# Kernel tuning notes

Measured on AMD Instinct MI355X. Metric: run time of the kernel, lower is better.

The kernel has to match this reference:

```python
import jax, jax.numpy as jnp
import numpy as np

N_NODES = 50000
N_EDGES = 640000
HIDDEN = 128


def setup_inputs() -> dict:
    key = jax.random.key(0)
    ks = jax.random.split(key, 8)
    z = jax.random.normal(ks[0], (N_NODES, HIDDEN), dtype=jnp.float32)
    sources = jax.random.randint(ks[1], (N_EDGES,), 0, N_NODES)
    dists = jax.random.randint(ks[2], (N_EDGES,), 0, N_NODES)
    weights = jax.random.uniform(ks[3], (N_EDGES, 1), dtype=jnp.float32)
    # nn.Linear-style params: W has shape [out, in]; we store transposed [in, out]
    s_msg = 1.0 / np.sqrt(2 * HIDDEN + 1)
    W_msg = jax.random.uniform(ks[4], (2 * HIDDEN + 1, HIDDEN), minval=-s_msg, maxval=s_msg, dtype=jnp.float32)
    b_msg = jax.random.uniform(ks[5], (HIDDEN,), minval=-s_msg, maxval=s_msg, dtype=jnp.float32)
    s_upd = 1.0 / np.sqrt(2 * HIDDEN)
    W_upd = jax.random.uniform(ks[6], (2 * HIDDEN, HIDDEN), minval=-s_upd, maxval=s_upd, dtype=jnp.float32)
    b_upd = jax.random.uniform(ks[7], (HIDDEN,), minval=-s_upd, maxval=s_upd, dtype=jnp.float32)
    return {"z": z, "sources": sources, "dists": dists, "weights": weights,
            "W_msg": W_msg, "b_msg": b_msg, "W_upd": W_upd, "b_upd": b_upd}


def reference(z, sources, dists, weights, W_msg, b_msg, W_upd, b_upd):
    n = z.shape[0]
    # gather -> concat -> message linear: [E, 2h+1] @ [2h+1, h]
    msg_input = jnp.concatenate([z[sources], z[dists], weights], axis=1)
    messages = msg_input @ W_msg + b_msg
    # scatter-amax aggregate into node buffers (empty nodes -> -inf -> 0)
    agg = jax.ops.segment_max(messages, dists, num_segments=n)
    agg = jnp.where(jnp.isinf(agg), 0.0, agg)
    # update linear on [n, 2h]
    return jnp.concatenate([z, agg], axis=1) @ W_upd + b_upd
```

## Files before the change

### kernel.cpp

```cpp
#include <hip/hip_runtime.h>

#define H 128
#define KSLOT 64
#define CSTRIDE 16

typedef __attribute__((ext_vector_type(8))) short bf8;
typedef __attribute__((ext_vector_type(8))) unsigned short u16x8;
typedef __attribute__((ext_vector_type(4))) float f32x4;

__device__ __forceinline__ unsigned short f2bf(float f) {
    unsigned u = __float_as_uint(f);
    return (unsigned short)((u + 0x7FFFu + ((u >> 16) & 1u)) >> 16);
}
__device__ __forceinline__ float bf2f(unsigned short b) {
    return __uint_as_float(((unsigned)b) << 16);
}

__global__ __launch_bounds__(256) void prep(
    const float* __restrict__ z, const float* __restrict__ Wmsg, const float* __restrict__ Wupd,
    unsigned short* __restrict__ zb,
    unsigned short* __restrict__ WmT,
    unsigned short* __restrict__ WuT,
    int* __restrict__ cnt,
    unsigned short* __restrict__ ZS,
    int N)
{
    const int t = blockIdx.x * 256 + threadIdx.x;
    const int n4 = (N * CSTRIDE) >> 2;
    if (t < n4) ((int4*)cnt)[t] = make_int4(0, 0, 0, 0);
    const int zi = t * 8;
    if (zi < N * H) {
        const float4* p = (const float4*)(z + zi);
        float4 v0 = p[0], v1 = p[1];
        ushort4 o0, o1;
        o0.x = f2bf(v0.x); o0.y = f2bf(v0.y); o0.z = f2bf(v0.z); o0.w = f2bf(v0.w);
        o1.x = f2bf(v1.x); o1.y = f2bf(v1.y); o1.z = f2bf(v1.z); o1.w = f2bf(v1.w);
        ushort4* q = (ushort4*)(zb + zi);
        q[0] = o0; q[1] = o1;
    }
    if (t < 16) {
        u16x8 s;
#pragma unroll
        for (int i = 0; i < 8; ++i) s[i] = 0xFF80;
        *(u16x8*)(ZS + (size_t)N * H + t * 8) = s;
    }
    if (t < 256 * H) {
        const int c = t >> 7, k = t & 127;
        WmT[t] = f2bf(Wmsg[(size_t)(k + (c & 128)) * H + (c & 127)]);
    }
    if (t < H * 256) {
        const int c = t >> 8, k = t & 255;
        WuT[t] = f2bf(Wupd[(size_t)k * H + c]);
    }
}

__global__ __launch_bounds__(256) void gemm1_scatter(
    const unsigned short* __restrict__ zb,
    const unsigned short* __restrict__ WmT,
    unsigned short* __restrict__ ZS,
    unsigned short* __restrict__ ZD,
    const int* __restrict__ src, const int* __restrict__ dst,
    const float* __restrict__ wgt, int* __restrict__ cnt,
    int2* __restrict__ ew,
    int N, int E, int ntiles, int ngemm)
{
    if ((int)blockIdx.x >= ngemm) {
        const int base = (blockIdx.x - ngemm) * 1024 + threadIdx.x;
        int dv[4], sv[4]; float wv[4]; bool ok[4];
#pragma unroll
        for (int k = 0; k < 4; ++k) {
            const int e = base + k * 256;
            ok[k] = e < E;
            const int ec = ok[k] ? e : 0;
            dv[k] = dst[ec]; sv[k] = src[ec]; wv[k] = wgt[ec];
        }
#pragma unroll
        for (int k = 0; k < 4; ++k) {
            if (ok[k]) {
                int p = atomicAdd(&cnt[(size_t)dv[k] * CSTRIDE], 1);
                if (p < KSLOT)
                    ew[((size_t)dv[k] << 6) + p] = make_int2(sv[k], __float_as_int(wv[k]));
            }
        }
        return;
    }
    const int l = threadIdx.x & 63;
    const int w = threadIdx.x >> 6;
    const int r = l & 15, g = l >> 4;
    const int colbase = w * 64;
    unsigned short* Out = (w < 2) ? ZS : ZD;
    const int outcol = colbase & 127;

    bf8 wf[4][4];
#pragma unroll
    for (int nf = 0; nf < 4; ++nf)
#pragma unroll
        for (int kk = 0; kk < 4; ++kk)
            wf[kk][nf] = *(const bf8*)(WmT + (size_t)(colbase + nf * 16 + r) * H + kk * 32 + g * 8);

    const f32x4 zero = {0.f, 0.f, 0.f, 0.f};
    for (int tt = blockIdx.x; tt < ntiles; tt += ngemm) {
        const int row0 = tt * 32;
#pragma unroll
        for (int m = 0; m < 2; ++m) {
            const int node = row0 + m * 16 + r;
            const int rowc = node < N ? node : N - 1;
            bf8 zf[4];
#pragma unroll
            for (int kk = 0; kk < 4; ++kk)
                zf[kk] = *(const bf8*)(zb + (size_t)rowc * H + kk * 32 + g * 8);
            f32x4 acc[4] = {zero, zero, zero, zero};
#pragma unroll
            for (int kk = 0; kk < 4; ++kk)
#pragma unroll
                for (int nf = 0; nf < 4; ++nf)
                    acc[nf] = __builtin_amdgcn_mfma_f32_16x16x32_bf16(wf[kk][nf], zf[kk], acc[nf], 0, 0, 0);
            if (node < N) {
#pragma unroll
                for (int nf = 0; nf < 4; ++nf) {
                    ushort4 o;
                    o.x = f2bf(acc[nf][0]); o.y = f2bf(acc[nf][1]);
                    o.z = f2bf(acc[nf][2]); o.w = f2bf(acc[nf][3]);
                    *(ushort4*)(Out + (size_t)node * H + outcol + nf * 16 + g * 4) = o;
                }
            }
        }
    }
}

__global__ __launch_bounds__(256) void aggregate(
    const unsigned short* __restrict__ ZS,
    const unsigned short* __restrict__ ZD,
    unsigned short* __restrict__ Agg,
    const float* __restrict__ bmsg, const float* __restrict__ wrow,
    const int* __restrict__ cnt, const int2* __restrict__ ew, int N)
{
    const int node = blockIdx.x * 4 + (threadIdx.x >> 6);
    if (node >= N) return;
    const int l = threadIdx.x & 63;
    const int sub = l >> 4;
    const int c16 = l & 15;

    const int d = min(cnt[(size_t)node * CSTRIDE], KSLOT);
    const int iters = (d + 7) >> 3;

    float wr[8];
    {
        float4 w0 = *(const float4*)(wrow + c16 * 8);
        float4 w1 = *(const float4*)(wrow + c16 * 8 + 4);
        wr[0] = w0.x; wr[1] = w0.y; wr[2] = w0.z; wr[3] = w0.w;
        wr[4] = w1.x; wr[5] = w1.y; wr[6] = w1.z; wr[7] = w1.w;
    }

    const float NINF = -__builtin_inff();
    float m[8];
#pragma unroll
    for (int i = 0; i < 8; ++i) m[i] = NINF;

    const int2* ep = ew + ((size_t)node << 6) + sub;
#pragma unroll 2
    for (int j = 0; j < iters; ++j) {
        const int s0 = j * 8 + sub, s1 = s0 + 4;
        int2 e0 = ep[j * 8];
        int2 e1 = ep[j * 8 + 4];
        const int r0 = (s0 < d) ? e0.x : N;
        const int r1 = (s1 < d) ? e1.x : N;
        const float w0 = (s0 < d) ? __int_as_float(e0.y) : 0.f;
        const float w1 = (s1 < d) ? __int_as_float(e1.y) : 0.f;
        u16x8 v0 = *(const u16x8*)(ZS + (size_t)r0 * H + c16 * 8);
        u16x8 v1 = *(const u16x8*)(ZS + (size_t)r1 * H + c16 * 8);
#pragma unroll
        for (int i = 0; i < 8; ++i)
            m[i] = fmaxf(m[i], __builtin_fmaf(w0, wr[i], bf2f((unsigned short)v0[i])));
#pragma unroll
        for (int i = 0; i < 8; ++i)
            m[i] = fmaxf(m[i], __builtin_fmaf(w1, wr[i], bf2f((unsigned short)v1[i])));
    }
#pragma unroll
    for (int i = 0; i < 8; ++i) {
        m[i] = fmaxf(m[i], __shfl_xor(m[i], 16));
        m[i] = fmaxf(m[i], __shfl_xor(m[i], 32));
    }

    if (sub == 0) {
        u16x8 zd = *(const u16x8*)(ZD + (size_t)node * H + c16 * 8);
        float bm[8];
        float4 b0 = *(const float4*)(bmsg + c16 * 8);
        float4 b1 = *(const float4*)(bmsg + c16 * 8 + 4);
        bm[0] = b0.x; bm[1] = b0.y; bm[2] = b0.z; bm[3] = b0.w;
        bm[4] = b1.x; bm[5] = b1.y; bm[6] = b1.z; bm[7] = b1.w;
        u16x8 o;
#pragma unroll
        for (int i = 0; i < 8; ++i) {
            float r = (d > 0) ? (m[i] + bf2f((unsigned short)zd[i]) + bm[i]) : 0.f;
            o[i] = f2bf(r);
        }
        *(u16x8*)(Agg + (size_t)node * H + c16 * 8) = o;
    }
}

__global__ __launch_bounds__(256) void gemm_upd_mfma(
    const unsigned short* __restrict__ zb,
    const unsigned short* __restrict__ Agg,
    const unsigned short* __restrict__ WuT,
    const float* __restrict__ bupd,
    float* __restrict__ out, int N, int ntiles)
{
    const int l = threadIdx.x & 63;
    const int w = threadIdx.x >> 6;
    const int r = l & 15, g = l >> 4;
    const int colbase = w * 32;

    bf8 wf[8][2];
#pragma unroll
    for (int nf = 0; nf < 2; ++nf)
#pragma unroll
        for (int kk = 0; kk < 8; ++kk)
            wf[kk][nf] = *(const bf8*)(WuT + (size_t)(colbase + nf * 16 + r) * 256 + kk * 32 + g * 8);
    float4 bias[2];
#pragma unroll
    for (int nf = 0; nf < 2; ++nf)
        bias[nf] = *(const float4*)(bupd + colbase + nf * 16 + g * 4);

    const f32x4 zero = {0.f, 0.f, 0.f, 0.f};
    for (int tt = blockIdx.x; tt < ntiles; tt += gridDim.x) {
        const int row0 = tt * 32;
#pragma unroll
        for (int m = 0; m < 2; ++m) {
            const int node = row0 + m * 16 + r;
            const int rowc = node < N ? node : N - 1;
            bf8 zf[8];
#pragma unroll
            for (int kk = 0; kk < 4; ++kk)
                zf[kk] = *(const bf8*)(zb + (size_t)rowc * H + kk * 32 + g * 8);
#pragma unroll
            for (int kk = 4; kk < 8; ++kk)
                zf[kk] = *(const bf8*)(Agg + (size_t)rowc * H + (kk - 4) * 32 + g * 8);
            f32x4 acc[2] = {zero, zero};
#pragma unroll
            for (int kk = 0; kk < 8; ++kk)
#pragma unroll
                for (int nf = 0; nf < 2; ++nf)
                    acc[nf] = __builtin_amdgcn_mfma_f32_16x16x32_bf16(wf[kk][nf], zf[kk], acc[nf], 0, 0, 0);
            if (node < N) {
#pragma unroll
                for (int nf = 0; nf < 2; ++nf) {
                    float4 o;
                    o.x = acc[nf][0] + bias[nf].x;
                    o.y = acc[nf][1] + bias[nf].y;
                    o.z = acc[nf][2] + bias[nf].z;
                    o.w = acc[nf][3] + bias[nf].w;
                    *(float4*)(out + (size_t)node * H + colbase + nf * 16 + g * 4) = o;
                }
            }
        }
    }
}

extern "C" void kernel_launch(void* const* d_in, const int* in_sizes, int n_in,
                              void* d_out, int out_size, void* d_ws, size_t ws_size,
                              hipStream_t stream) {
    const float* z    = (const float*)d_in[0];
    const int*   src  = (const int*)d_in[1];
    const int*   dst  = (const int*)d_in[2];
    const float* wgt  = (const float*)d_in[3];
    const float* Wmsg = (const float*)d_in[4];
    const float* bmsg = (const float*)d_in[5];
    const float* Wupd = (const float*)d_in[6];
    const float* bupd = (const float*)d_in[7];
    float* out = (float*)d_out;

    const int N = in_sizes[0] / H;
    const int E = in_sizes[1];
    const int Npad = ((N + 31) / 32) * 32;
    const int ntiles = Npad / 32;

    unsigned short* zb  = (unsigned short*)d_ws;
    unsigned short* ZS  = zb + (size_t)Npad * H;
    unsigned short* ZD  = ZS + (size_t)(Npad + 32) * H;
    unsigned short* Agg = ZD + (size_t)Npad * H;
    unsigned short* WmT = Agg + (size_t)Npad * H;
    unsigned short* WuT = WmT + 256 * H;
    int*  cnt = (int*)(WuT + H * 256);
    int2* ew  = (int2*)(cnt + (size_t)N * CSTRIDE);

    const int ngemm = 784;
    const int nscat = (E + 1023) / 1024;
    const int nprep_threads = max(N * H / 8, (N * CSTRIDE) / 4);
    const int nprep = (nprep_threads + 255) / 256;

    prep<<<nprep, 256, 0, stream>>>(z, Wmsg, Wupd, zb, WmT, WuT, cnt, ZS, N);

    gemm1_scatter<<<ngemm + nscat, 256, 0, stream>>>(
        zb, WmT, ZS, ZD, src, dst, wgt, cnt, ew, N, E, ntiles, ngemm);

    aggregate<<<(N + 3) / 4, 256, 0, stream>>>(
        ZS, ZD, Agg, bmsg, Wmsg + (size_t)256 * H, cnt, ew, N);

    gemm_upd_mfma<<<784, 256, 0, stream>>>(zb, Agg, WuT, bupd, out, N, ntiles);
}
```

Baseline: 117.9 us.

## Replace per-node atomic slot scatter with counting-sort edge partition and LDS tile aggregation

The per-node atomic counter and fixed 64-slot edge buckets are replaced by a chunked histogram over 64-node tiles, split into 4 sub-bins by node index modulo 4. Two scan kernels and a partition kernel then write the edges into a compact sorted array, packing the source index and local destination into one int. A tile_agg kernel has each wave walk its sub-bin and keep per-node maxima in shared memory before applying the bias and the ZD term. This removes the global atomics, the per-node degree cap and the sentinel row, in exchange for four extra launches, a one-block scan, and narrower 4-byte gathers with fewer edges in flight per wave.

Measured after the change: 152.0 us. 1.29x slower.

```diff
diff --git a/kernel.cpp b/kernel.cpp
--- a/kernel.cpp
+++ b/kernel.cpp
@@ -1,8 +1,8 @@
 #include <hip/hip_runtime.h>
 
 #define H 128
-#define KSLOT 64
-#define CSTRIDE 16
+#define CHUNK 4096
+#define MAXB 3200
 
 typedef __attribute__((ext_vector_type(8))) short bf8;
 typedef __attribute__((ext_vector_type(8))) unsigned short u16x8;
@@ -21,13 +21,9 @@
     unsigned short* __restrict__ zb,
     unsigned short* __restrict__ WmT,
     unsigned short* __restrict__ WuT,
-    int* __restrict__ cnt,
-    unsigned short* __restrict__ ZS,
     int N)
 {
     const int t = blockIdx.x * 256 + threadIdx.x;
-    const int n4 = (N * CSTRIDE) >> 2;
-    if (t < n4) ((int4*)cnt)[t] = make_int4(0, 0, 0, 0);
     const int zi = t * 8;
     if (zi < N * H) {
         const float4* p = (const float4*)(z + zi);
@@ -38,12 +34,6 @@
         ushort4* q = (ushort4*)(zb + zi);
         q[0] = o0; q[1] = o1;
     }
-    if (t < 16) {
-        u16x8 s;
-#pragma unroll
-        for (int i = 0; i < 8; ++i) s[i] = 0xFF80;
-        *(u16x8*)(ZS + (size_t)N * H + t * 8) = s;
-    }
     if (t < 256 * H) {
         const int c = t >> 7, k = t & 127;
         WmT[t] = f2bf(Wmsg[(size_t)(k + (c & 128)) * H + (c & 127)]);
@@ -54,36 +44,13 @@
     }
 }
 
-__global__ __launch_bounds__(256) void gemm1_scatter(
+__global__ __launch_bounds__(256) void gemm1(
     const unsigned short* __restrict__ zb,
     const unsigned short* __restrict__ WmT,
     unsigned short* __restrict__ ZS,
     unsigned short* __restrict__ ZD,
-    const int* __restrict__ src, const int* __restrict__ dst,
-    const float* __restrict__ wgt, int* __restrict__ cnt,
-    int2* __restrict__ ew,
-    int N, int E, int ntiles, int ngemm)
-{
-    if ((int)blockIdx.x >= ngemm) {
-        const int base = (blockIdx.x - ngemm) * 1024 + threadIdx.x;
-        int dv[4], sv[4]; float wv[4]; bool ok[4];
-#pragma unroll
-        for (int k = 0; k < 4; ++k) {
-            const int e = base + k * 256;
-            ok[k] = e < E;
-            const int ec = ok[k] ? e : 0;
-            dv[k] = dst[ec]; sv[k] = src[ec]; wv[k] = wgt[ec];
-        }
-#pragma unroll
-        for (int k = 0; k < 4; ++k) {
-            if (ok[k]) {
-                int p = atomicAdd(&cnt[(size_t)dv[k] * CSTRIDE], 1);
-                if (p < KSLOT)
-                    ew[((size_t)dv[k] << 6) + p] = make_int2(sv[k], __float_as_int(wv[k]));
-            }
-        }
-        return;
-    }
+    int N, int ntiles)
+{
     const int l = threadIdx.x & 63;
     const int w = threadIdx.x >> 6;
     const int r = l & 15, g = l >> 4;
@@ -99,7 +66,7 @@
             wf[kk][nf] = *(const bf8*)(WmT + (size_t)(colbase + nf * 16 + r) * H + kk * 32 + g * 8);
 
     const f32x4 zero = {0.f, 0.f, 0.f, 0.f};
-    for (int tt = blockIdx.x; tt < ntiles; tt += ngemm) {
+    for (int tt = blockIdx.x; tt < ntiles; tt += gridDim.x) {
         const int row0 = tt * 32;
 #pragma unroll
         for (int m = 0; m < 2; ++m) {
@@ -128,74 +95,161 @@
     }
 }
 
-__global__ __launch_bounds__(256) void aggregate(
+__global__ __launch_bounds__(256) void hist_tiles(
+    const int* __restrict__ dst, int* __restrict__ histG, int E, int NT4)
+{
+    __shared__ int h[MAXB];
+    for (int i = threadIdx.x; i < NT4; i += 256) h[i] = 0;
+    __syncthreads();
+    const int e0 = blockIdx.x * CHUNK;
+#pragma unroll
+    for (int j = 0; j < CHUNK / 256; ++j) {
+        const int e = e0 + j * 256 + threadIdx.x;
+        if (e < E) {
+            const int d = dst[e];
+            atomicAdd(&h[(d >> 6) * 4 + (d & 3)], 1);
+        }
+    }
+    __syncthreads();
+    for (int i = threadIdx.x; i < NT4; i += 256)
+        histG[(size_t)blockIdx.x * NT4 + i] = h[i];
+}
+
+__global__ __launch_bounds__(256) void scan_bins(
+    int* __restrict__ histG, int* __restrict__ tileTot, int NB, int NT4)
+{
+    __shared__ int sh[256];
+    const int b = blockIdx.x;
+    const int t = threadIdx.x;
+    int v = (t < NB) ? histG[(size_t)t * NT4 + b] : 0;
+    sh[t] = v;
+    __syncthreads();
+#pragma unroll
+    for (int off = 1; off < 256; off <<= 1) {
+        int x = (t >= off) ? sh[t - off] : 0;
+        __syncthreads();
+        sh[t] += x;
+        __syncthreads();
+    }
+    if (t < NB) histG[(size_t)t * NT4 + b] = sh[t] - v;
+    if (t == 255) tileTot[b] = sh[255];
+}
+
+__global__ __launch_bounds__(256) void scan_total(
+    const int* __restrict__ tileTot, int* __restrict__ tileBase, int NT4)
+{
+    __shared__ int sh[256];
+    const int t = threadIdx.x;
+    const int PER = (NT4 + 255) / 256;
+    int loc[16];
+    int s = 0;
+    for (int j = 0; j < PER; ++j) {
+        const int i = t * PER + j;
+        const int v = (i < NT4) ? tileTot[i] : 0;
+        loc[j] = s; s += v;
+    }
+    sh[t] = s;
+    __syncthreads();
+#pragma unroll
+    for (int off = 1; off < 256; off <<= 1) {
+        int x = (t >= off) ? sh[t - off] : 0;
+        __syncthreads();
+        sh[t] += x;
+        __syncthreads();
+    }
+    const int base = sh[t] - s;
+    for (int j = 0; j < PER; ++j) {
+        const int i = t * PER + j;
+        if (i < NT4) tileBase[i] = base + loc[j];
+    }
+}
+
+__global__ __launch_bounds__(256) void partition_edges(
+    const int* __restrict__ src, const int* __restrict__ dst, const float* __restrict__ wgt,
+    const int* __restrict__ histG, const int* __restrict__ tileBase,
+    int2* __restrict__ EP, int E, int NT4)
+{
+    __shared__ int c[MAXB];
+    for (int i = threadIdx.x; i < NT4; i += 256) c[i] = 0;
+    __syncthreads();
+    const int e0 = blockIdx.x * CHUNK;
+    const size_t hbase = (size_t)blockIdx.x * NT4;
+#pragma unroll
+    for (int j = 0; j < CHUNK / 256; ++j) {
+        const int e = e0 + j * 256 + threadIdx.x;
+        if (e < E) {
+            const int d = dst[e];
+            const int b = (d >> 6) * 4 + (d & 3);
+            const int r = atomicAdd(&c[b], 1);
+            const int slot = tileBase[b] + histG[hbase + b] + r;
+            EP[slot] = make_int2(src[e] | ((d & 63) << 16), __float_as_int(wgt[e]));
+        }
+    }
+}
+
+__global__ __launch_bounds__(256) void tile_agg(
     const unsigned short* __restrict__ ZS,
     const unsigned short* __restrict__ ZD,
     unsigned short* __restrict__ Agg,
     const float* __restrict__ bmsg, const float* __restrict__ wrow,
-    const int* __restrict__ cnt, const int2* __restrict__ ew, int N)
-{
-    const int node = blockIdx.x * 4 + (threadIdx.x >> 6);
-    if (node >= N) return;
-    const int l = threadIdx.x & 63;
-    const int sub = l >> 4;
-    const int c16 = l & 15;
-
-    const int d = min(cnt[(size_t)node * CSTRIDE], KSLOT);
-    const int iters = (d + 7) >> 3;
-
-    float wr[8];
-    {
-        float4 w0 = *(const float4*)(wrow + c16 * 8);
-        float4 w1 = *(const float4*)(wrow + c16 * 8 + 4);
-        wr[0] = w0.x; wr[1] = w0.y; wr[2] = w0.z; wr[3] = w0.w;
-        wr[4] = w1.x; wr[5] = w1.y; wr[6] = w1.z; wr[7] = w1.w;
-    }
-
+    const int* __restrict__ tileBase, const int* __restrict__ tileTot,
+    const int2* __restrict__ EP, int N)
+{
+    __shared__ float agg[64][132];
+    const int t = blockIdx.x;
+    const int w = threadIdx.x >> 6;
+    const int lane = threadIdx.x & 63;
+
+    for (int i = threadIdx.x; i < 64 * 132; i += 256)
+        ((float*)agg)[i] = -__builtin_inff();
+    __syncthreads();
+
+    const float wr0 = wrow[2 * lane], wr1 = wrow[2 * lane + 1];
+    const int b = t * 4 + w;
+    int p = tileBase[b];
+    const int pe = p + tileTot[b];
+
+#define PROC(rr, qq)                                                         \
+    {                                                                        \
+        const int dl = (rr.x >> 16) & 63;                                    \
+        const float ww = __int_as_float(rr.y);                               \
+        const float v0 = __builtin_fmaf(ww, wr0, bf2f((unsigned short)(qq & 0xFFFF))); \
+        const float v1 = __builtin_fmaf(ww, wr1, bf2f((unsigned short)(qq >> 16)));    \
+        float2* ap = (float2*)&agg[dl][2 * lane];                            \
+        float2 cc = *ap;                                                     \
+        cc.x = fmaxf(cc.x, v0); cc.y = fmaxf(cc.y, v1);                      \
+        *ap = cc;                                                            \
+    }
+
+    for (; p + 4 <= pe; p += 4) {
+        const int2 r0 = EP[p], r1 = EP[p + 1], r2 = EP[p + 2], r3 = EP[p + 3];
+        const unsigned q0 = *(const unsigned*)(ZS + (size_t)(r0.x & 0xFFFF) * H + 2 * lane);
+        const unsigned q1 = *(const unsigned*)(ZS + (size_t)(r1.x & 0xFFFF) * H + 2 * lane);
+        const unsigned q2 = *(const unsigned*)(ZS + (size_t)(r2.x & 0xFFFF) * H + 2 * lane);
+        const unsigned q3 = *(const unsigned*)(ZS + (size_t)(r3.x & 0xFFFF) * H + 2 * lane);
+        PROC(r0, q0); PROC(r1, q1); PROC(r2, q2); PROC(r3, q3);
+    }
+    for (; p < pe; ++p) {
+        const int2 r = EP[p];
+        const unsigned q = *(const unsigned*)(ZS + (size_t)(r.x & 0xFFFF) * H + 2 * lane);
+        PROC(r, q);
+    }
+#undef PROC
+    __syncthreads();
+
+    const float bm0 = bmsg[2 * lane], bm1 = bmsg[2 * lane + 1];
     const float NINF = -__builtin_inff();
-    float m[8];
-#pragma unroll
-    for (int i = 0; i < 8; ++i) m[i] = NINF;
-
-    const int2* ep = ew + ((size_t)node << 6) + sub;
-#pragma unroll 2
-    for (int j = 0; j < iters; ++j) {
-        const int s0 = j * 8 + sub, s1 = s0 + 4;
-        int2 e0 = ep[j * 8];
-        int2 e1 = ep[j * 8 + 4];
-        const int r0 = (s0 < d) ? e0.x : N;
-        const int r1 = (s1 < d) ? e1.x : N;
-        const float w0 = (s0 < d) ? __int_as_float(e0.y) : 0.f;
-        const float w1 = (s1 < d) ? __int_as_float(e1.y) : 0.f;
-        u16x8 v0 = *(const u16x8*)(ZS + (size_t)r0 * H + c16 * 8);
-        u16x8 v1 = *(const u16x8*)(ZS + (size_t)r1 * H + c16 * 8);
-#pragma unroll
-        for (int i = 0; i < 8; ++i)
-            m[i] = fmaxf(m[i], __builtin_fmaf(w0, wr[i], bf2f((unsigned short)v0[i])));
-#pragma unroll
-        for (int i = 0; i < 8; ++i)
-            m[i] = fmaxf(m[i], __builtin_fmaf(w1, wr[i], bf2f((unsigned short)v1[i])));
-    }
-#pragma unroll
-    for (int i = 0; i < 8; ++i) {
-        m[i] = fmaxf(m[i], __shfl_xor(m[i], 16));
-        m[i] = fmaxf(m[i], __shfl_xor(m[i], 32));
-    }
-
-    if (sub == 0) {
-        u16x8 zd = *(const u16x8*)(ZD + (size_t)node * H + c16 * 8);
-        float bm[8];
-        float4 b0 = *(const float4*)(bmsg + c16 * 8);
-        float4 b1 = *(const float4*)(bmsg + c16 * 8 + 4);
-        bm[0] = b0.x; bm[1] = b0.y; bm[2] = b0.z; bm[3] = b0.w;
-        bm[4] = b1.x; bm[5] = b1.y; bm[6] = b1.z; bm[7] = b1.w;
-        u16x8 o;
-#pragma unroll
-        for (int i = 0; i < 8; ++i) {
-            float r = (d > 0) ? (m[i] + bf2f((unsigned short)zd[i]) + bm[i]) : 0.f;
-            o[i] = f2bf(r);
-        }
-        *(u16x8*)(Agg + (size_t)node * H + c16 * 8) = o;
+    for (int i = 0; i < 16; ++i) {
+        const int n = w + 4 * i;
+        const int g = t * 64 + n;
+        if (g < N) {
+            const float a0 = agg[n][2 * lane], a1 = agg[n][2 * lane + 1];
+            const unsigned zd = *(const unsigned*)(ZD + (size_t)g * H + 2 * lane);
+            const float o0 = (a0 == NINF) ? 0.f : a0 + bf2f((unsigned short)(zd & 0xFFFF)) + bm0;
+            const float o1 = (a1 == NINF) ? 0.f : a1 + bf2f((unsigned short)(zd >> 16)) + bm1;
+            const unsigned ou = (unsigned)f2bf(o0) | ((unsigned)f2bf(o1) << 16);
+            *(unsigned*)(Agg + (size_t)g * H + 2 * lane) = ou;
+        }
     }
 }
 
@@ -274,28 +328,34 @@
     const int E = in_sizes[1];
     const int Npad = ((N + 31) / 32) * 32;
     const int ntiles = Npad / 32;
-
-    unsigned short* zb  = (unsigned short*)d_ws;
-    unsigned short* ZS  = zb + (size_t)Npad * H;
-    unsigned short* ZD  = ZS + (size_t)(Npad + 32) * H;
-    unsigned short* Agg = ZD + (size_t)Npad * H;
-    unsigned short* WmT = Agg + (size_t)Npad * H;
-    unsigned short* WuT = WmT + 256 * H;
-    int*  cnt = (int*)(WuT + H * 256);
-    int2* ew  = (int2*)(cnt + (size_t)N * CSTRIDE);
-
-    const int ngemm = 784;
-    const int nscat = (E + 1023) / 1024;
-    const int nprep_threads = max(N * H / 8, (N * CSTRIDE) / 4);
-    const int nprep = (nprep_threads + 255) / 256;
-
-    prep<<<nprep, 256, 0, stream>>>(z, Wmsg, Wupd, zb, WmT, WuT, cnt, ZS, N);
-
-    gemm1_scatter<<<ngemm + nscat, 256, 0, stream>>>(
-        zb, WmT, ZS, ZD, src, dst, wgt, cnt, ew, N, E, ntiles, ngemm);
-
-    aggregate<<<(N + 3) / 4, 256, 0, stream>>>(
-        ZS, ZD, Agg, bmsg, Wmsg + (size_t)256 * H, cnt, ew, N);
+    const int NT  = (N + 63) >> 6;
+    const int NT4 = NT * 4;
+    const int NB  = (E + CHUNK - 1) / CHUNK;
+
+    unsigned short* zb   = (unsigned short*)d_ws;
+    unsigned short* ZS   = zb + (size_t)Npad * H;
+    unsigned short* ZD   = ZS + (size_t)Npad * H;
+    unsigned short* Agg  = ZD + (size_t)Npad * H;
+    unsigned short* WmT  = Agg + (size_t)Npad * H;
+    unsigned short* WuT  = WmT + 256 * H;
+    int*  histG    = (int*)(WuT + H * 256);
+    int*  tileTot  = histG + (size_t)NB * NT4;
+    int*  tileBase = tileTot + NT4;
+    int2* EP       = (int2*)(tileBase + NT4);
+
+    const int nprep = (N * H / 8 + 255) / 256;
+
+    prep<<<nprep, 256, 0, stream>>>(z, Wmsg, Wupd, zb, WmT, WuT, N);
+
+    gemm1<<<784, 256, 0, stream>>>(zb, WmT, ZS, ZD, N, ntiles);
+
+    hist_tiles<<<NB, 256, 0, stream>>>(dst, histG, E, NT4);
+    scan_bins<<<NT4, 256, 0, stream>>>(histG, tileTot, NB, NT4);
+    scan_total<<<1, 256, 0, stream>>>(tileTot, tileBase, NT4);
+    partition_edges<<<NB, 256, 0, stream>>>(src, dst, wgt, histG, tileBase, EP, E, NT4);
+
+    tile_agg<<<NT, 256, 0, stream>>>(ZS, ZD, Agg, bmsg, Wmsg + (size_t)256 * H,
+                                     tileBase, tileTot, EP, N);
 
     gemm_upd_mfma<<<784, 256, 0, stream>>>(zb, Agg, WuT, bupd, out, N, ntiles);
 }
```
